# Kernel tuning notes

Measured on AMD Instinct MI355X. Metric: run time of the kernel, lower is better.

## Reference

```python
import jax, jax.numpy as jnp
import numpy as np

D = 1024
H = 16
HD = D // H  # 64
S = 2048
B = 1


def setup_inputs() -> dict:
    key = jax.random.key(0)
    ks = jax.random.split(key, 6)
    return {
        "GLO": jax.random.normal(ks[0], (B, S, D), dtype=jnp.float32),
        "LOC": jax.random.normal(ks[1], (B, S, D), dtype=jnp.float32),
        "W_q": jax.random.normal(ks[2], (H, D, HD), dtype=jnp.float32),
        "W_k": jax.random.normal(ks[3], (H, D, HD), dtype=jnp.float32),
        "W_v": jax.random.normal(ks[4], (H, D, HD), dtype=jnp.float32),
        "W_o": jax.random.normal(ks[5], (H * HD, D), dtype=jnp.float32),
    }


def _cross_attn(q_src, kv_src, W_q, W_k, W_v, W_o):
    # q_src: [B,Sq,D], kv_src: [B,Sk,D]
    b, sq, _ = q_src.shape
    Q = jnp.einsum('bsd,hde->bhse', q_src, W_q)   # [B,H,Sq,hd]
    K = jnp.einsum('bsd,hde->bhse', kv_src, W_k)  # [B,H,Sk,hd]
    V = jnp.einsum('bsd,hde->bhse', kv_src, W_v)  # [B,H,Sk,hd]
    scores = jnp.einsum('bhqe,bhke->bhqk', Q, K) / jnp.sqrt(jnp.float32(HD))
    weights = jax.nn.softmax(scores, axis=-1)
    out = jnp.einsum('bhqk,bhke->bhqe', weights, V)  # [B,H,Sq,hd]
    # Faithful to torch .view (raw memory reinterpretation, no head transpose)
    out = out.reshape(b, sq, H * HD)
    return out @ W_o  # [B,Sq,D]


def reference(GLO, LOC, W_q, W_k, W_v, W_o):
    GLO_prime = _cross_attn(GLO, LOC, W_q, W_k, W_v, W_o)
    LOC_prime = _cross_attn(LOC, GLO, W_q, W_k, W_v, W_o)
    return (GLO_prime, LOC_prime)
```

## Files before the change

kernel.cpp:

```cpp
#include <hip/hip_runtime.h>
#include <math.h>

#define S_LEN 2048
#define D_DIM 1024
#define NH 16
#define HD 64

typedef __attribute__((ext_vector_type(8))) short bf16x8;
typedef __attribute__((ext_vector_type(4))) float f32x4;

#define MFMA(a, b, c) __builtin_amdgcn_mfma_f32_16x16x32_bf16((a), (b), (c), 0, 0, 0)

__device__ __forceinline__ unsigned short f2bf(float x) {
    unsigned int u = __float_as_uint(x);
    u = (u + 0x7FFFu + ((u >> 16) & 1u)) >> 16;
    return (unsigned short)u;
}
__device__ __forceinline__ float bf2f(unsigned short b) {
    return __uint_as_float(((unsigned int)b) << 16);
}
__device__ __forceinline__ void gl_lds16(const void* g, void* l) {
    __builtin_amdgcn_global_load_lds((const __attribute__((address_space(1))) unsigned int*)g,
                                     (__attribute__((address_space(3))) unsigned int*)l, 16, 0, 0);
}

#if defined(__has_builtin)
#if __has_builtin(__builtin_amdgcn_cvt_pk_bf16_f32)
#define HAVE_CVT_PK_BF16 1
#endif
#endif
__device__ __forceinline__ unsigned pack_bf16(float a, float b) {
#ifdef HAVE_CVT_PK_BF16
    auto r = __builtin_amdgcn_cvt_pk_bf16_f32(a, b);
    unsigned u;
    __builtin_memcpy(&u, &r, 4);
    return u;
#else
    unsigned ua = __float_as_uint(a) + 0x8000u;
    unsigned ub = __float_as_uint(b) + 0x8000u;
    return __builtin_amdgcn_perm(ub, ua, 0x07060302u);
#endif
}


__global__ __launch_bounds__(256) void prep(const float* __restrict__ GLO,
                                            const float* __restrict__ LOC,
                                            const float* __restrict__ Wq,
                                            const float* __restrict__ Wk,
                                            const float* __restrict__ Wv,
                                            const float* __restrict__ Wo,
                                            unsigned short* __restrict__ Xh,
                                            unsigned short* __restrict__ Xl,
                                            unsigned short* __restrict__ Wqh,
                                            unsigned short* __restrict__ Wql,
                                            unsigned short* __restrict__ Wkh,
                                            unsigned short* __restrict__ Wkl,
                                            unsigned short* __restrict__ Wvt,
                                            unsigned short* __restrict__ Wot) {
    int idx = blockIdx.x * 256 + threadIdx.x;
    if (idx < (1 << 19)) {
        int gg = idx & 7;
        int row = (idx >> 3) & 127;
        int kblk = (idx >> 10) & 15;
        int r = (idx >> 14) * 128 + row;
        int kg = gg ^ (row & 7);
        const float* src = (r & 2048) ? LOC : GLO;
        const float* sp = src + (size_t)(r & 2047) * 1024 + kblk * 64 + kg * 8;
        float4 x0 = *(const float4*)sp;
        float4 x1 = *(const float4*)(sp + 4);
        size_t t = (size_t)idx * 8;
        ushort4 h0, l0, h1, l1;
        h0.x = f2bf(x0.x); l0.x = f2bf(x0.x - bf2f(h0.x));
        h0.y = f2bf(x0.y); l0.y = f2bf(x0.y - bf2f(h0.y));
        h0.z = f2bf(x0.z); l0.z = f2bf(x0.z - bf2f(h0.z));
        h0.w = f2bf(x0.w); l0.w = f2bf(x0.w - bf2f(h0.w));
        h1.x = f2bf(x1.x); l1.x = f2bf(x1.x - bf2f(h1.x));
        h1.y = f2bf(x1.y); l1.y = f2bf(x1.y - bf2f(h1.y));
        h1.z = f2bf(x1.z); l1.z = f2bf(x1.z - bf2f(h1.z));
        h1.w = f2bf(x1.w); l1.w = f2bf(x1.w - bf2f(h1.w));
        *(ushort4*)(Xh + t) = h0;
        *(ushort4*)(Xh + t + 4) = h1;
        *(ushort4*)(Xl + t) = l0;
        *(ushort4*)(Xl + t + 4) = l1;
    } else {
        int idx2 = idx - (1 << 19);
        int sec = idx2 >> 17;
        int j = idx2 & 0x1FFFF;
        size_t t = (size_t)j * 8;
        if (sec < 3) {
            int gg = j & 7;
            int e = (j >> 3) & 63;
            int kblk = (j >> 9) & 15;
            int head = j >> 13;
            int kg = gg ^ (e & 7);
            int d0 = kblk * 64 + kg * 8;
            const float* W = (sec == 0) ? Wq : (sec == 1) ? Wk : Wv;
            const float* wp = W + (size_t)head * 65536 + (size_t)d0 * 64 + e;
            float wv8[8];
#pragma unroll
            for (int i = 0; i < 8; ++i) wv8[i] = wp[i * 64];
            if (sec == 0) {
                ushort4 h0, l0, h1, l1;
#pragma unroll
                for (int i = 0; i < 8; ++i) {
                    float v = wv8[i] * 0.18033688011112042f;
                    unsigned short hi = f2bf(v);
                    unsigned short lo = f2bf(v - bf2f(hi));
                    if (i < 4) {
                        ((unsigned short*)&h0)[i] = hi;
                        ((unsigned short*)&l0)[i] = lo;
                    } else {
                        ((unsigned short*)&h1)[i - 4] = hi;
                        ((unsigned short*)&l1)[i - 4] = lo;
                    }
                }
                *(ushort4*)(Wqh + t) = h0;
                *(ushort4*)(Wqh + t + 4) = h1;
                *(ushort4*)(Wql + t) = l0;
                *(ushort4*)(Wql + t + 4) = l1;
            } else if (sec == 1) {
                ushort4 h0, l0, h1, l1;
#pragma unroll
                for (int i = 0; i < 8; ++i) {
                    float v = wv8[i];
                    unsigned short hi = f2bf(v);
                    unsigned short lo = f2bf(v - bf2f(hi));
                    if (i < 4) {
                        ((unsigned short*)&h0)[i] = hi;
                        ((unsigned short*)&l0)[i] = lo;
                    } else {
                        ((unsigned short*)&h1)[i - 4] = hi;
                        ((unsigned short*)&l1)[i - 4] = lo;
                    }
                }
                *(ushort4*)(Wkh + t) = h0;
                *(ushort4*)(Wkh + t + 4) = h1;
                *(ushort4*)(Wkl + t) = l0;
                *(ushort4*)(Wkl + t + 4) = l1;
            } else {
                ushort4 v0, v1;
#pragma unroll
                for (int i = 0; i < 8; ++i) {
                    unsigned short b = f2bf(wv8[i]);
                    if (i < 4)
                        ((unsigned short*)&v0)[i] = b;
                    else
                        ((unsigned short*)&v1)[i - 4] = b;
                }
                *(ushort4*)(Wvt + t) = v0;
                *(ushort4*)(Wvt + t + 4) = v1;
            }
        } else {
            int gg = j & 7;
            int col = (j >> 3) & 63;
            int kblk = (j >> 9) & 15;
            int nblk = j >> 13;
            int kg = gg ^ (col & 7);
            int k0 = kblk * 64 + kg * 8;
            int n = nblk * 64 + col;
            ushort4 v0, v1;
#pragma unroll
            for (int i = 0; i < 8; ++i) {
                unsigned short b = f2bf(Wo[(size_t)(k0 + i) * 1024 + n]);
                if (i < 4)
                    ((unsigned short*)&v0)[i] = b;
                else
                    ((unsigned short*)&v1)[i - 4] = b;
            }
            *(ushort4*)(Wot + t) = v0;
            *(ushort4*)(Wot + t + 4) = v1;
        }
    }
}

__global__ __launch_bounds__(256) void qkv_proj(const unsigned short* __restrict__ Xh,
                                                const unsigned short* __restrict__ Xl,
                                                const unsigned short* __restrict__ Wqh,
                                                const unsigned short* __restrict__ Wql,
                                                const unsigned short* __restrict__ Wkh,
                                                const unsigned short* __restrict__ Wkl,
                                                const unsigned short* __restrict__ Wvt,
                                                unsigned short* __restrict__ Qh,
                                                unsigned short* __restrict__ Ql,
                                                unsigned short* __restrict__ Kh,
                                                unsigned short* __restrict__ Kl,
                                                unsigned short* __restrict__ Vt) {
    __shared__ unsigned short lds[36864];
    const int bid = blockIdx.x;
    const int mblk = bid & 31;
    const int head = bid >> 5;
    const int tid = threadIdx.x;
    const int lane = tid & 63;
    const int w = tid >> 6;
    const int l15 = lane & 15, quad = lane >> 4;

    f32x4 aq[2][4] = {}, ak[2][4] = {}, av[2][4] = {};
    const size_t abase0 = (size_t)mblk * 131072;
    const size_t bbase0 = (size_t)head * 65536;

    for (int kb = 0; kb < 16; ++kb) {
        __syncthreads();
        {
            const size_t ab = abase0 + (size_t)kb * 8192;
            const size_t bb = bbase0 + (size_t)kb * 4096;
#pragma unroll
            for (int j = 0; j < 4; ++j) {
                int seg = j * 256 + tid;
                gl_lds16(Xh + ab + seg * 8, &lds[seg * 8]);
                gl_lds16(Xl + ab + seg * 8, &lds[8192 + seg * 8]);
            }
#pragma unroll
            for (int j = 0; j < 2; ++j) {
                int seg = j * 256 + tid;
                gl_lds16(Wqh + bb + seg * 8, &lds[16384 + seg * 8]);
                gl_lds16(Wql + bb + seg * 8, &lds[20480 + seg * 8]);
                gl_lds16(Wkh + bb + seg * 8, &lds[24576 + seg * 8]);
                gl_lds16(Wkl + bb + seg * 8, &lds[28672 + seg * 8]);
                gl_lds16(Wvt + bb + seg * 8, &lds[32768 + seg * 8]);
            }
        }
        __syncthreads();

#pragma unroll
        for (int ksub = 0; ksub < 2; ++ksub) {
            bf16x8 ah[2], al8[2];
#pragma unroll
            for (int mt = 0; mt < 2; ++mt) {
                int row = w * 32 + mt * 16 + l15;
                int g = (ksub * 4 + quad) ^ (row & 7);
                ah[mt] = *(const bf16x8*)&lds[row * 64 + g * 8];
                al8[mt] = *(const bf16x8*)&lds[8192 + row * 64 + g * 8];
            }
#pragma unroll
            for (int nt = 0; nt < 4; ++nt) {
                int col = nt * 16 + l15;
                int o = col * 64 + ((ksub * 4 + quad) ^ (col & 7)) * 8;
                bf16x8 bqh = *(const bf16x8*)&lds[16384 + o];
                bf16x8 bql = *(const bf16x8*)&lds[20480 + o];
                bf16x8 bkh = *(const bf16x8*)&lds[24576 + o];
                bf16x8 bkl = *(const bf16x8*)&lds[28672 + o];
                bf16x8 bv = *(const bf16x8*)&lds[32768 + o];
#pragma unroll
                for (int mt = 0; mt < 2; ++mt) {
                    f32x4 a = aq[mt][nt];
                    a = MFMA(ah[mt], bqh, a);
                    a = MFMA(ah[mt], bql, a);
                    a = MFMA(al8[mt], bqh, a);
                    aq[mt][nt] = a;
                    f32x4 b = ak[mt][nt];
                    b = MFMA(ah[mt], bkh, b);
                    b = MFMA(ah[mt], bkl, b);
                    b = MFMA(al8[mt], bkh, b);
                    ak[mt][nt] = b;
                    av[mt][nt] = MFMA(ah[mt], bv, av[mt][nt]);
                }
            }
        }
    }

#pragma unroll
    for (int mt = 0; mt < 2; ++mt) {
        const int rbase = mblk * 128 + w * 32 + mt * 16 + quad * 4;
#pragma unroll
        for (int nt = 0; nt < 4; ++nt) {
            const int col = head * 64 + nt * 16 + l15;
#pragma unroll
            for (int r = 0; r < 4; ++r) {
                size_t a = (size_t)(rbase + r) * D_DIM + col;
                float vq = aq[mt][nt][r];
                unsigned short hq = f2bf(vq);
                Qh[a] = hq;
                Ql[a] = f2bf(vq - bf2f(hq));
                float vk = ak[mt][nt][r];
                unsigned short hk = f2bf(vk);
                Kh[a] = hk;
                Kl[a] = f2bf(vk - bf2f(hk));
            }
            ushort4 vp;
            vp.x = f2bf(av[mt][nt][0]);
            vp.y = f2bf(av[mt][nt][1]);
            vp.z = f2bf(av[mt][nt][2]);
            vp.w = f2bf(av[mt][nt][3]);
            *(ushort4*)(Vt + (size_t)col * (2 * S_LEN) + rbase) = vp;
        }
    }
}

__global__ __launch_bounds__(512, 4) void attn_kernel(const unsigned short* __restrict__ Qh_,
                                                      const unsigned short* __restrict__ Ql_,
                                                      const unsigned short* __restrict__ Kh_,
                                                      const unsigned short* __restrict__ Kl_,
                                                      const unsigned short* __restrict__ Vt_,
                                                      unsigned short* __restrict__ Oatt) {
    __shared__ unsigned short lds[32768];
    const int bid = blockIdx.x;
    const int qblk = bid & 15;
    const int head = (bid >> 4) & 15;
    const int dir = bid >> 8;
    const int src_q = dir, src_kv = 1 - dir;

    const int tid = threadIdx.x;
    const int lane = tid & 63;
    const int w = tid >> 6;
    const int l15 = lane & 15, quad = lane >> 4;
    const int q0w = qblk * 128 + w * 16;

    const unsigned short* KhB0 = Kh_ + (size_t)(src_kv * S_LEN) * D_DIM + head * 64;
    const unsigned short* KlB0 = Kl_ + (size_t)(src_kv * S_LEN) * D_DIM + head * 64;
    const unsigned short* Vtp = Vt_ + (size_t)(head * 64) * (2 * S_LEN) + src_kv * S_LEN;

    const int i0 = tid;
    const int sr0 = i0 >> 3, sc0 = ((i0 & 7) ^ (sr0 & 7)) * 8;

    auto stage = [&](int k0, int boff) {
        const unsigned short* KhB = KhB0 + (size_t)k0 * D_DIM;
        const unsigned short* KlB = KlB0 + (size_t)k0 * D_DIM;
        const unsigned short* VB = Vtp + k0;
        gl_lds16(KhB + (size_t)sr0 * D_DIM + sc0, &lds[boff + i0 * 8]);
        gl_lds16(KlB + (size_t)sr0 * D_DIM + sc0, &lds[boff + 4096 + i0 * 8]);
        gl_lds16(VB + (size_t)sr0 * (2 * S_LEN) + sc0, &lds[boff + 8192 + i0 * 8]);
    };

    bf16x8 qh[2], ql[2];
    {
        const size_t qrow = (size_t)(src_q * S_LEN + q0w + l15) * D_DIM + head * 64 + quad * 8;
#pragma unroll
        for (int c = 0; c < 2; ++c) {
            qh[c] = *(const bf16x8*)(Qh_ + qrow + c * 32);
            ql[c] = *(const bf16x8*)(Ql_ + qrow + c * 32);
        }
    }

    bf16x8 ones_;
#pragma unroll
    for (int i = 0; i < 8; ++i) ones_[i] = (short)0x3F80;

    f32x4 o[4] = {};
    f32x4 li = {};
    float mi = -1e30f;
    unsigned short* Pw = lds + 24576 + w * 1024;

    auto chunk = [&](int kb) {
        f32x4 sa[4];
#pragma unroll
        for (int kt = 0; kt < 4; ++kt) {
            const int row = kt * 16 + l15;
            const int s0 = (quad ^ (row & 7)) * 8;
            const int s1 = ((4 + quad) ^ (row & 7)) * 8;
            bf16x8 kh0 = *(const bf16x8*)&lds[kb + row * 64 + s0];
            bf16x8 kh1 = *(const bf16x8*)&lds[kb + row * 64 + s1];
            bf16x8 kl0 = *(const bf16x8*)&lds[kb + 4096 + row * 64 + s0];
            bf16x8 kl1 = *(const bf16x8*)&lds[kb + 4096 + row * 64 + s1];
            f32x4 a = {};
            a = MFMA(kh0, qh[0], a);
            a = MFMA(kh1, qh[1], a);
            a = MFMA(kl0, qh[0], a);
            a = MFMA(kl1, qh[1], a);
            a = MFMA(kh0, ql[0], a);
            a = MFMA(kh1, ql[1], a);
            sa[kt] = a;
        }

        f32x4 t4 = __builtin_elementwise_max(__builtin_elementwise_max(sa[0], sa[1]),
                                             __builtin_elementwise_max(sa[2], sa[3]));
        float tm = fmaxf(fmaxf(t4[0], t4[1]), fmaxf(t4[2], t4[3]));
        tm = fmaxf(tm, __shfl_xor(tm, 16, 64));
        tm = fmaxf(tm, __shfl_xor(tm, 32, 64));
        if (__ballot(tm > mi)) {
            float mn = fmaxf(mi, tm);
            float al = exp2f(mi - mn);
            mi = mn;
            const f32x4 alv = {al, al, al, al};
            li *= alv;
#pragma unroll
            for (int et = 0; et < 4; ++et) o[et] *= alv;
        }
        const f32x4 mnv = {mi, mi, mi, mi};
#pragma unroll
        for (int kt = 0; kt < 4; ++kt) {
            f32x4 p = sa[kt] - mnv;
#pragma unroll
            for (int r = 0; r < 4; ++r) p[r] = exp2f(p[r]);
            uint2 pk;
            pk.x = pack_bf16(p[0], p[1]);
            pk.y = pack_bf16(p[2], p[3]);
            int g = (kt * 2 + (quad >> 1)) ^ (l15 & 7);
            *(uint2*)&Pw[l15 * 64 + g * 8 + (quad & 1) * 4] = pk;
        }

#pragma unroll
        for (int c = 0; c < 2; ++c) {
            bf16x8 pf = *(const bf16x8*)&Pw[l15 * 64 + (((c * 4 + quad) ^ (l15 & 7)) * 8)];
            li = MFMA(ones_, pf, li);
#pragma unroll
            for (int et = 0; et < 4; ++et) {
                const int row = et * 16 + l15;
                const int sl = ((c * 4 + quad) ^ (row & 7)) * 8;
                bf16x8 vf = *(const bf16x8*)&lds[kb + 8192 + row * 64 + sl];
                o[et] = MFMA(vf, pf, o[et]);
            }
        }
    };

    stage(0, 0);
#pragma unroll 1
    for (int kd = 0; kd < 32; kd += 2) {
        __syncthreads();
        if (kd + 1 < 32) stage((kd + 1) * 64, 12288);
        chunk(0);
        __syncthreads();
        if (kd + 2 < 32) stage((kd + 2) * 64, 0);
        chunk(12288);
    }

    const size_t obase = (size_t)(dir * 16 + head) * 131072 + (size_t)l15 * 8192;
    {
        float rl = __builtin_amdgcn_rcpf(li[0]);
        const int rowit = qblk * 8 + w;
#pragma unroll
        for (int et = 0; et < 4; ++et) {
            int g = ((et * 2 + (quad >> 1)) ^ (rowit & 7)) & 7;
            ushort4 pk;
            pk.x = f2bf(o[et][0] * rl);
            pk.y = f2bf(o[et][1] * rl);
            pk.z = f2bf(o[et][2] * rl);
            pk.w = f2bf(o[et][3] * rl);
            *(ushort4*)(Oatt + obase + (size_t)rowit * 64 + g * 8 + (quad & 1) * 4) = pk;
        }
    }
}

__global__ __launch_bounds__(256) void oproj(const unsigned short* __restrict__ Oatt,
                                             const unsigned short* __restrict__ Wot,
                                             float* __restrict__ out) {
    __shared__ unsigned short lds[24576];
    const int bid = blockIdx.x;
    const int nblk = bid & 15;
    const int mblk = bid >> 4;
    const int tid = threadIdx.x;
    const int lane = tid & 63, w = tid >> 6, l15 = lane & 15, quad = lane >> 4;

    f32x4 acc[2][4] = {};
    const size_t abase = (size_t)mblk * 131072;
    const size_t bbase = (size_t)nblk * 65536;

    auto ostage = [&](int kb, int boff) {
#pragma unroll
        for (int j = 0; j < 4; ++j) {
            int seg = j * 256 + tid;
            gl_lds16(Oatt + abase + (size_t)kb * 8192 + seg * 8, &lds[boff + seg * 8]);
        }
#pragma unroll
        for (int j = 0; j < 2; ++j) {
            int seg = j * 256 + tid;
            gl_lds16(Wot + bbase + (size_t)kb * 4096 + seg * 8, &lds[boff + 8192 + seg * 8]);
        }
    };

    auto compute = [&](int boff) {
#pragma unroll
        for (int ksub = 0; ksub < 2; ++ksub) {
            bf16x8 a[2];
#pragma unroll
            for (int mt = 0; mt < 2; ++mt) {
                int row = w * 32 + mt * 16 + l15;
                a[mt] =
                    *(const bf16x8*)&lds[boff + row * 64 + (((ksub * 4 + quad) ^ (row & 7)) * 8)];
            }
#pragma unroll
            for (int nt = 0; nt < 4; ++nt) {
                int col = nt * 16 + l15;
                bf16x8 b = *(const bf16x8*)&lds[boff + 8192 + col * 64 +
                                                (((ksub * 4 + quad) ^ (col & 7)) * 8)];
#pragma unroll
                for (int mt = 0; mt < 2; ++mt) acc[mt][nt] = MFMA(a[mt], b, acc[mt][nt]);
            }
        }
    };

    ostage(0, 0);
#pragma unroll 1
    for (int kb = 0; kb < 16; kb += 2) {
        __syncthreads();
        if (kb + 1 < 16) ostage(kb + 1, 12288);
        compute(0);
        __syncthreads();
        if (kb + 2 < 16) ostage(kb + 2, 0);
        compute(12288);
    }

#pragma unroll
    for (int mt = 0; mt < 2; ++mt) {
        const int rbase = mblk * 128 + w * 32 + mt * 16 + quad * 4;
#pragma unroll
        for (int nt = 0; nt < 4; ++nt)
#pragma unroll
            for (int r = 0; r < 4; ++r)
                out[(size_t)(rbase + r) * D_DIM + nblk * 64 + nt * 16 + l15] = acc[mt][nt][r];
    }
}

extern "C" void kernel_launch(void* const* d_in, const int* in_sizes, int n_in, void* d_out,
                              int out_size, void* d_ws, size_t ws_size, hipStream_t stream) {
    const float* GLO = (const float*)d_in[0];
    const float* LOC = (const float*)d_in[1];
    const float* Wq = (const float*)d_in[2];
    const float* Wk = (const float*)d_in[3];
    const float* Wv = (const float*)d_in[4];
    const float* Wo = (const float*)d_in[5];
    float* out = (float*)d_out;

    unsigned short* ws = (unsigned short*)d_ws;
    unsigned short* Xh = ws + 0;
    unsigned short* Xl = ws + 4194304;
    unsigned short* Wqh = ws + 8388608;
    unsigned short* Wql = ws + 9437184;
    unsigned short* Wkh = ws + 10485760;
    unsigned short* Wkl = ws + 11534336;
    unsigned short* Wvt = ws + 12582912;
    unsigned short* Wot = ws + 13631488;
    unsigned short* Qh = ws + 14680064;
    unsigned short* Ql = ws + 18874368;
    unsigned short* Kh = ws + 23068672;
    unsigned short* Kl = ws + 27262976;
    unsigned short* Vt = ws + 31457280;
    unsigned short* Oatt = ws + 35651584;

    prep<<<4096, 256, 0, stream>>>(GLO, LOC, Wq, Wk, Wv, Wo, Xh, Xl, Wqh, Wql, Wkh, Wkl, Wvt, Wot);
    qkv_proj<<<512, 256, 0, stream>>>(Xh, Xl, Wqh, Wql, Wkh, Wkl, Wvt, Qh, Ql, Kh, Kl, Vt);
    attn_kernel<<<512, 512, 0, stream>>>(Qh, Ql, Kh, Kl, Vt, Oatt);
    oproj<<<512, 256, 0, stream>>>(Oatt, Wot, out);
}
```

Baseline: 246.3 us.

## Halve attention KV tile to 32 keys, raise occupancy, compute row sums in registers

The attention kernel now stages 32-key chunks instead of 64. This halves shared memory and doubles the launch-bounds minimum block count so more workgroups fit per CU. The softmax denominator is accumulated in scalar registers with a final cross-lane shuffle reduction instead of a ones-vector MFMA per chunk, and the MFMA issue order is interleaved with the LDS loads. The trade-off is twice as many loop iterations and barriers, plus smaller MFMA batches per sync.

```diff
diff --git a/kernel.cpp b/kernel.cpp
--- a/kernel.cpp
+++ b/kernel.cpp
@@ -286,13 +286,13 @@
     }
 }
 
-__global__ __launch_bounds__(512, 4) void attn_kernel(const unsigned short* __restrict__ Qh_,
+__global__ __launch_bounds__(512, 8) void attn_kernel(const unsigned short* __restrict__ Qh_,
                                                       const unsigned short* __restrict__ Ql_,
                                                       const unsigned short* __restrict__ Kh_,
                                                       const unsigned short* __restrict__ Kl_,
                                                       const unsigned short* __restrict__ Vt_,
                                                       unsigned short* __restrict__ Oatt) {
-    __shared__ unsigned short lds[32768];
+    __shared__ unsigned short lds[16384];
     const int bid = blockIdx.x;
     const int qblk = bid & 15;
     const int head = (bid >> 4) & 15;
@@ -309,16 +309,19 @@
     const unsigned short* KlB0 = Kl_ + (size_t)(src_kv * S_LEN) * D_DIM + head * 64;
     const unsigned short* Vtp = Vt_ + (size_t)(head * 64) * (2 * S_LEN) + src_kv * S_LEN;
 
-    const int i0 = tid;
-    const int sr0 = i0 >> 3, sc0 = ((i0 & 7) ^ (sr0 & 7)) * 8;
+    const int segK = tid & 255;
+    const int rowK = segK >> 3, gK = segK & 7;
+    const int colK = (gK ^ (rowK & 7)) * 8;
+    const unsigned short* kbase = (tid < 256 ? KhB0 : KlB0) + (size_t)rowK * D_DIM + colK;
+    const int ldsK = (tid < 256 ? 0 : 2048) + segK * 8;
+    const int rowV = segK >> 2, gV = segK & 3;
+    const int colV = (gV ^ (rowV & 3)) * 8;
+    const unsigned short* vbase = Vtp + (size_t)rowV * (2 * S_LEN) + colV;
+    const int ldsV = 4096 + segK * 8;
 
     auto stage = [&](int k0, int boff) {
-        const unsigned short* KhB = KhB0 + (size_t)k0 * D_DIM;
-        const unsigned short* KlB = KlB0 + (size_t)k0 * D_DIM;
-        const unsigned short* VB = Vtp + k0;
-        gl_lds16(KhB + (size_t)sr0 * D_DIM + sc0, &lds[boff + i0 * 8]);
-        gl_lds16(KlB + (size_t)sr0 * D_DIM + sc0, &lds[boff + 4096 + i0 * 8]);
-        gl_lds16(VB + (size_t)sr0 * (2 * S_LEN) + sc0, &lds[boff + 8192 + i0 * 8]);
+        gl_lds16(kbase + (size_t)k0 * D_DIM, &lds[boff + ldsK]);
+        if (tid < 256) gl_lds16(vbase + k0, &lds[boff + ldsV]);
     };
 
     bf16x8 qh[2], ql[2];
@@ -331,38 +334,33 @@
         }
     }
 
-    bf16x8 ones_;
-#pragma unroll
-    for (int i = 0; i < 8; ++i) ones_[i] = (short)0x3F80;
-
     f32x4 o[4] = {};
-    f32x4 li = {};
     float mi = -1e30f;
-    unsigned short* Pw = lds + 24576 + w * 1024;
+    float lip = 0.f;
+    unsigned short* Pw = lds + 12288 + w * 512;
 
     auto chunk = [&](int kb) {
-        f32x4 sa[4];
-#pragma unroll
-        for (int kt = 0; kt < 4; ++kt) {
+        f32x4 sa[2];
+#pragma unroll
+        for (int kt = 0; kt < 2; ++kt) {
             const int row = kt * 16 + l15;
             const int s0 = (quad ^ (row & 7)) * 8;
             const int s1 = ((4 + quad) ^ (row & 7)) * 8;
+            f32x4 a = {};
             bf16x8 kh0 = *(const bf16x8*)&lds[kb + row * 64 + s0];
+            a = MFMA(kh0, qh[0], a);
+            a = MFMA(kh0, ql[0], a);
             bf16x8 kh1 = *(const bf16x8*)&lds[kb + row * 64 + s1];
-            bf16x8 kl0 = *(const bf16x8*)&lds[kb + 4096 + row * 64 + s0];
-            bf16x8 kl1 = *(const bf16x8*)&lds[kb + 4096 + row * 64 + s1];
-            f32x4 a = {};
-            a = MFMA(kh0, qh[0], a);
             a = MFMA(kh1, qh[1], a);
+            a = MFMA(kh1, ql[1], a);
+            bf16x8 kl0 = *(const bf16x8*)&lds[kb + 2048 + row * 64 + s0];
             a = MFMA(kl0, qh[0], a);
+            bf16x8 kl1 = *(const bf16x8*)&lds[kb + 2048 + row * 64 + s1];
             a = MFMA(kl1, qh[1], a);
-            a = MFMA(kh0, ql[0], a);
-            a = MFMA(kh1, ql[1], a);
             sa[kt] = a;
         }
 
-        f32x4 t4 = __builtin_elementwise_max(__builtin_elementwise_max(sa[0], sa[1]),
-                                             __builtin_elementwise_max(sa[2], sa[3]));
+        f32x4 t4 = __builtin_elementwise_max(sa[0], sa[1]);
         float tm = fmaxf(fmaxf(t4[0], t4[1]), fmaxf(t4[2], t4[3]));
         tm = fmaxf(tm, __shfl_xor(tm, 16, 64));
         tm = fmaxf(tm, __shfl_xor(tm, 32, 64));
@@ -370,52 +368,54 @@
             float mn = fmaxf(mi, tm);
             float al = exp2f(mi - mn);
             mi = mn;
+            lip *= al;
             const f32x4 alv = {al, al, al, al};
-            li *= alv;
 #pragma unroll
             for (int et = 0; et < 4; ++et) o[et] *= alv;
         }
         const f32x4 mnv = {mi, mi, mi, mi};
-#pragma unroll
-        for (int kt = 0; kt < 4; ++kt) {
+        f32x4 rs4 = {};
+#pragma unroll
+        for (int kt = 0; kt < 2; ++kt) {
             f32x4 p = sa[kt] - mnv;
 #pragma unroll
             for (int r = 0; r < 4; ++r) p[r] = exp2f(p[r]);
+            rs4 += p;
             uint2 pk;
             pk.x = pack_bf16(p[0], p[1]);
             pk.y = pack_bf16(p[2], p[3]);
-            int g = (kt * 2 + (quad >> 1)) ^ (l15 & 7);
-            *(uint2*)&Pw[l15 * 64 + g * 8 + (quad & 1) * 4] = pk;
-        }
-
-#pragma unroll
-        for (int c = 0; c < 2; ++c) {
-            bf16x8 pf = *(const bf16x8*)&Pw[l15 * 64 + (((c * 4 + quad) ^ (l15 & 7)) * 8)];
-            li = MFMA(ones_, pf, li);
-#pragma unroll
-            for (int et = 0; et < 4; ++et) {
-                const int row = et * 16 + l15;
-                const int sl = ((c * 4 + quad) ^ (row & 7)) * 8;
-                bf16x8 vf = *(const bf16x8*)&lds[kb + 8192 + row * 64 + sl];
-                o[et] = MFMA(vf, pf, o[et]);
-            }
+            int g = (kt * 2 + (quad >> 1)) ^ (l15 & 3);
+            *(uint2*)&Pw[l15 * 32 + g * 8 + (quad & 1) * 4] = pk;
+        }
+        lip += (rs4[0] + rs4[1]) + (rs4[2] + rs4[3]);
+
+        bf16x8 pf = *(const bf16x8*)&Pw[l15 * 32 + ((quad ^ (l15 & 3)) * 8)];
+#pragma unroll
+        for (int et = 0; et < 4; ++et) {
+            const int row = et * 16 + l15;
+            const int sl = (quad ^ (row & 3)) * 8;
+            bf16x8 vf = *(const bf16x8*)&lds[kb + 4096 + row * 32 + sl];
+            o[et] = MFMA(vf, pf, o[et]);
         }
     };
 
     stage(0, 0);
 #pragma unroll 1
-    for (int kd = 0; kd < 32; kd += 2) {
+    for (int kd = 0; kd < 64; kd += 2) {
         __syncthreads();
-        if (kd + 1 < 32) stage((kd + 1) * 64, 12288);
+        if (kd + 1 < 64) stage((kd + 1) * 32, 6144);
         chunk(0);
         __syncthreads();
-        if (kd + 2 < 32) stage((kd + 2) * 64, 0);
-        chunk(12288);
+        if (kd + 2 < 64) stage((kd + 2) * 32, 0);
+        chunk(6144);
     }
 
     const size_t obase = (size_t)(dir * 16 + head) * 131072 + (size_t)l15 * 8192;
     {
-        float rl = __builtin_amdgcn_rcpf(li[0]);
+        float lq = lip;
+        lq += __shfl_xor(lq, 16, 64);
+        lq += __shfl_xor(lq, 32, 64);
+        float rl = __builtin_amdgcn_rcpf(lq);
         const int rowit = qblk * 8 + w;
 #pragma unroll
         for (int et = 0; et < 4; ++et) {
```

After: 288.5 us. +17.2%, slower.
